# Optimization experiments

Hardware: AMD Instinct MI355X
Metric: run time of the kernel (lower is better)

Reference implementation:

```python
import jax, jax.numpy as jnp
import numpy as np
from jax import lax

SIGMA_D = 120.0
SIGMA_R = 1.2
WINDOW = 3
PAD = WINDOW // 2


def _sobel_kernels():
    smooth = jnp.array([1.0, 2.0, 1.0], dtype=jnp.float32) / 4.0
    deriv = jnp.array([1.0, 0.0, -1.0], dtype=jnp.float32)
    Kh = jnp.einsum('i,j,k->ijk', deriv, smooth, smooth)
    Kw = jnp.einsum('i,j,k->ijk', smooth, deriv, smooth)
    Kd = jnp.einsum('i,j,k->ijk', smooth, smooth, deriv)
    # (O=3, I=1, 3, 3, 3)
    return jnp.stack([Kh, Kw, Kd], axis=0)[:, None]


def _spatial_weights():
    r = np.arange(-PAD, PAD + 1)
    offs = np.stack(np.meshgrid(r, r, r, indexing='ij'), axis=-1).reshape(-1, 3).astype(np.float32)
    dist_sq = (offs ** 2).sum(axis=1)
    return jnp.asarray(np.exp(-dist_sq / (2.0 * SIGMA_D ** 2)))


def setup_inputs() -> dict:
    key = jax.random.key(0)
    volume = jax.random.normal(key, (1, 1, 96, 96, 96), dtype=jnp.float32)
    return {"volume": volume}


def reference(volume):
    B, C, D, H, W = volume.shape
    kernels = _sobel_kernels()
    # Sobel gradient, SAME (zero) padding like F.conv3d(padding=1): (B,3,D,H,W)
    grad = lax.conv_general_dilated(
        volume, kernels, window_strides=(1, 1, 1), padding=[(1, 1)] * 3,
        dimension_numbers=('NCDHW', 'OIDHW', 'NCDHW'))

    pad_cfg = ((0, 0), (0, 0), (PAD, PAD), (PAD, PAD), (PAD, PAD))
    vol_pad = jnp.pad(volume, pad_cfg, mode='edge')
    grad_pad = jnp.pad(grad, pad_cfg, mode='edge')

    offsets = [(dh, dw, dd) for dh in range(WINDOW) for dw in range(WINDOW) for dd in range(WINDOW)]
    # (B, K, D, H, W)
    neighbor_vals = jnp.stack(
        [vol_pad[:, 0, dh:dh + D, dw:dw + H, dd:dd + W] for (dh, dw, dd) in offsets], axis=1)
    # (B, K, 3, D, H, W)
    neighbor_grads = jnp.stack(
        [grad_pad[:, :, dh:dh + D, dw:dw + H, dd:dd + W] for (dh, dw, dd) in offsets], axis=1)

    # ||grad_p - grad_q||^2 over the 3 gradient channels; gaussian on the norm
    # equals exp(-||.||^2 / (2 sigma_r^2)) directly (sqrt then square cancels).
    grad_diff_sq = ((grad[:, None] - neighbor_grads) ** 2).sum(axis=2)  # (B,K,D,H,W)
    range_weights = jnp.exp(-grad_diff_sq / (2.0 * SIGMA_R ** 2))

    sw = _spatial_weights().reshape(1, -1, 1, 1, 1)
    weights = sw * range_weights
    numerator = (weights * neighbor_vals).sum(axis=1, keepdims=True)
    denominator = jnp.clip(weights.sum(axis=1, keepdims=True), 1e-8, None)
    return numerator / denominator
```

## Files before the change

### kernel.cpp

```cpp
#include <hip/hip_runtime.h>


#define NV 96
#define NV2 (NV * NV)

#define TX 32
#define TY 4
#define TZ 4
#define VX (TX + 4)
#define VY (TY + 4)
#define VZ (TZ + 4)
#define GX (TX + 2)
#define GY (TY + 2)
#define GZ (TZ + 2)
#define NVOL (VX * VY * VZ)

__global__ __launch_bounds__(256) void fused_bilateral_kernel(
    const float* __restrict__ vol, float* __restrict__ out) {
    __shared__ float sv[VZ][VY][VX];
    __shared__ float4 sq[GZ][GY][GX];

    const int X0 = blockIdx.x * TX;
    const int Y0 = blockIdx.y * TY;
    const int Z0 = blockIdx.z * TZ;
    const int t = threadIdx.x;

    for (int li = t; li < NVOL; li += 256) {
        int lx = li % VX;
        int lyz = li / VX;
        int ly = lyz % VY;
        int lz = lyz / VY;
        int gx = X0 - 2 + lx;
        int gy = Y0 - 2 + ly;
        int gz = Z0 - 2 + lz;
        float v = 0.0f;
        if (gx >= 0 && gx < NV && gy >= 0 && gy < NV && gz >= 0 && gz < NV)
            v = vol[gz * NV2 + gy * NV + gx];
        sv[lz][ly][lx] = v;
    }
    __syncthreads();

    if (t < GX * GY) {
        const int gx_ = t % GX;
        const int gy_ = t / GX;
        float s0 = 0.f, s1 = 0.f, s2 = 0.f;
        float w0 = 0.f, w1 = 0.f, w2 = 0.f;
        float u0 = 0.f, u1 = 0.f, u2 = 0.f;
        float v11p = 0.f;
#pragma unroll
        for (int p = 0; p < VZ; ++p) {
            float a00 = sv[p][gy_ + 0][gx_ + 0];
            float a01 = sv[p][gy_ + 0][gx_ + 1];
            float a02 = sv[p][gy_ + 0][gx_ + 2];
            float a10 = sv[p][gy_ + 1][gx_ + 0];
            float a11 = sv[p][gy_ + 1][gx_ + 1];
            float a12 = sv[p][gy_ + 1][gx_ + 2];
            float a20 = sv[p][gy_ + 2][gx_ + 0];
            float a21 = sv[p][gy_ + 2][gx_ + 1];
            float a22 = sv[p][gy_ + 2][gx_ + 2];
            float r0 = 0.25f * a00 + 0.5f * a01 + 0.25f * a02;
            float r1 = 0.25f * a10 + 0.5f * a11 + 0.25f * a12;
            float r2 = 0.25f * a20 + 0.5f * a21 + 0.25f * a22;
            float sxy = 0.25f * r0 + 0.5f * r1 + 0.25f * r2;
            float dyx = r0 - r2;
            float dx0 = a00 - a02;
            float dx1 = a10 - a12;
            float dx2 = a20 - a22;
            float dxs = 0.25f * dx0 + 0.5f * dx1 + 0.25f * dx2;
            s0 = s1; s1 = s2; s2 = sxy;
            w0 = w1; w1 = w2; w2 = dyx;
            u0 = u1; u1 = u2; u2 = dxs;
            if (p >= 2) {
                float gh = s0 - s2;
                float gw = 0.25f * w0 + 0.5f * w1 + 0.25f * w2;
                float gd = 0.25f * u0 + 0.5f * u1 + 0.25f * u2;
                sq[p - 2][gy_][gx_] = make_float4(gh, gw, gd, v11p);
            }
            v11p = a11;
        }
    }
    __syncthreads();

    const int tx = t & 31;
    const int ty = (t >> 5) & 3;
    const int tzh = t >> 7;

    const float inv2sd = 1.0f / (2.0f * 120.0f * 120.0f);
    const float inv2sr = 1.0f / (2.0f * 1.2f * 1.2f);

    const int ox = X0 + tx;
    const int oy = Y0 + ty;
    const int oz0 = Z0 + tzh;
    const int oz1 = oz0 + 2;

    const float4 c0 = sq[tzh + 1][ty + 1][tx + 1];
    const float4 c1 = sq[tzh + 3][ty + 1][tx + 1];

    int nx[3], ny[3], nz[5];
#pragma unroll
    for (int d = 0; d < 3; ++d) {
        nx[d] = min(max(ox + d - 1, 0), NV - 1) - (X0 - 1);
        ny[d] = min(max(oy + d - 1, 0), NV - 1) - (Y0 - 1);
    }
#pragma unroll
    for (int p = 0; p < 5; ++p)
        nz[p] = min(max(oz0 + p - 1, 0), NV - 1) - (Z0 - 1);

    float num0 = 0.0f, den0 = 0.0f, num1 = 0.0f, den1 = 0.0f;

#pragma unroll
    for (int p = 0; p < 5; ++p) {
#pragma unroll
        for (int iy = 0; iy < 3; ++iy) {
#pragma unroll
            for (int ix = 0; ix < 3; ++ix) {
                float4 q = sq[nz[p]][ny[iy]][nx[ix]];
                if (p <= 2) {
                    const float sdc =
                        (float)((p - 1) * (p - 1) + (iy - 1) * (iy - 1) +
                                (ix - 1) * (ix - 1)) * inv2sd;
                    float a = c0.x - q.x, b = c0.y - q.y, e = c0.z - q.z;
                    float g = a * a + b * b + e * e;
                    float w = __expf(-(sdc + g * inv2sr));
                    num0 += w * q.w;
                    den0 += w;
                }
                if (p >= 2) {
                    const float sdc =
                        (float)((p - 3) * (p - 3) + (iy - 1) * (iy - 1) +
                                (ix - 1) * (ix - 1)) * inv2sd;
                    float a = c1.x - q.x, b = c1.y - q.y, e = c1.z - q.z;
                    float g = a * a + b * b + e * e;
                    float w = __expf(-(sdc + g * inv2sr));
                    num1 += w * q.w;
                    den1 += w;
                }
            }
        }
    }

    out[oz0 * NV2 + oy * NV + ox] = num0 / fmaxf(den0, 1e-8f);
    out[oz1 * NV2 + oy * NV + ox] = num1 / fmaxf(den1, 1e-8f);
}

extern "C" void kernel_launch(void* const* d_in, const int* in_sizes, int n_in,
                              void* d_out, int out_size, void* d_ws, size_t ws_size,
                              hipStream_t stream) {
    const float* vol = (const float*)d_in[0];
    float* out = (float*)d_out;

    dim3 grid(NV / TX, NV / TY, NV / TZ);
    fused_bilateral_kernel<<<grid, dim3(256), 0, stream>>>(vol, out);
}
```

Baseline: 71.20 us.

## Enlarge tile to 32x8x4 and compute four z-outputs per thread

Doubles the tile height so each 256-thread block covers 32x8x4 outputs. Each thread now walks a 6-deep z column of the gradient tile and accumulates four outputs, reusing each shared-memory neighbour load across up to three outputs. It also folds the spatial constant into a single fma feeding a raw exp2 intrinsic, and splits the gradient-column stage into a loop because 340 columns exceed the block size. This cuts halo overhead and LDS reads per output, at the cost of more shared memory and registers per block and half as many blocks.

After: 77.11 us. 1.08x slower.

```diff
diff --git a/kernel.cpp b/kernel.cpp
--- a/kernel.cpp
+++ b/kernel.cpp
@@ -5,7 +5,7 @@
 #define NV2 (NV * NV)
 
 #define TX 32
-#define TY 4
+#define TY 8
 #define TZ 4
 #define VX (TX + 4)
 #define VY (TY + 4)
@@ -14,6 +14,9 @@
 #define GY (TY + 2)
 #define GZ (TZ + 2)
 #define NVOL (VX * VY * VZ)
+#define NCOL (GX * GY)
+
+#define LOG2E 1.44269504088896340736f
 
 __global__ __launch_bounds__(256) void fused_bilateral_kernel(
     const float* __restrict__ vol, float* __restrict__ out) {
@@ -40,107 +43,107 @@
     }
     __syncthreads();
 
-    if (t < GX * GY) {
-        const int gx_ = t % GX;
-        const int gy_ = t / GX;
-        float s0 = 0.f, s1 = 0.f, s2 = 0.f;
-        float w0 = 0.f, w1 = 0.f, w2 = 0.f;
-        float u0 = 0.f, u1 = 0.f, u2 = 0.f;
-        float v11p = 0.f;
 #pragma unroll
-        for (int p = 0; p < VZ; ++p) {
-            float a00 = sv[p][gy_ + 0][gx_ + 0];
-            float a01 = sv[p][gy_ + 0][gx_ + 1];
-            float a02 = sv[p][gy_ + 0][gx_ + 2];
-            float a10 = sv[p][gy_ + 1][gx_ + 0];
-            float a11 = sv[p][gy_ + 1][gx_ + 1];
-            float a12 = sv[p][gy_ + 1][gx_ + 2];
-            float a20 = sv[p][gy_ + 2][gx_ + 0];
-            float a21 = sv[p][gy_ + 2][gx_ + 1];
-            float a22 = sv[p][gy_ + 2][gx_ + 2];
-            float r0 = 0.25f * a00 + 0.5f * a01 + 0.25f * a02;
-            float r1 = 0.25f * a10 + 0.5f * a11 + 0.25f * a12;
-            float r2 = 0.25f * a20 + 0.5f * a21 + 0.25f * a22;
-            float sxy = 0.25f * r0 + 0.5f * r1 + 0.25f * r2;
-            float dyx = r0 - r2;
-            float dx0 = a00 - a02;
-            float dx1 = a10 - a12;
-            float dx2 = a20 - a22;
-            float dxs = 0.25f * dx0 + 0.5f * dx1 + 0.25f * dx2;
-            s0 = s1; s1 = s2; s2 = sxy;
-            w0 = w1; w1 = w2; w2 = dyx;
-            u0 = u1; u1 = u2; u2 = dxs;
-            if (p >= 2) {
-                float gh = s0 - s2;
-                float gw = 0.25f * w0 + 0.5f * w1 + 0.25f * w2;
-                float gd = 0.25f * u0 + 0.5f * u1 + 0.25f * u2;
-                sq[p - 2][gy_][gx_] = make_float4(gh, gw, gd, v11p);
+    for (int base = 0; base < NCOL; base += 256) {
+        int li = base + t;
+        if (li < NCOL) {
+            const int gx_ = li % GX;
+            const int gy_ = li / GX;
+            float s0 = 0.f, s1 = 0.f, s2 = 0.f;
+            float w0 = 0.f, w1 = 0.f, w2 = 0.f;
+            float u0 = 0.f, u1 = 0.f, u2 = 0.f;
+            float v11p = 0.f;
+#pragma unroll
+            for (int p = 0; p < VZ; ++p) {
+                float a00 = sv[p][gy_ + 0][gx_ + 0];
+                float a01 = sv[p][gy_ + 0][gx_ + 1];
+                float a02 = sv[p][gy_ + 0][gx_ + 2];
+                float a10 = sv[p][gy_ + 1][gx_ + 0];
+                float a11 = sv[p][gy_ + 1][gx_ + 1];
+                float a12 = sv[p][gy_ + 1][gx_ + 2];
+                float a20 = sv[p][gy_ + 2][gx_ + 0];
+                float a21 = sv[p][gy_ + 2][gx_ + 1];
+                float a22 = sv[p][gy_ + 2][gx_ + 2];
+                float r0 = 0.25f * a00 + 0.5f * a01 + 0.25f * a02;
+                float r1 = 0.25f * a10 + 0.5f * a11 + 0.25f * a12;
+                float r2 = 0.25f * a20 + 0.5f * a21 + 0.25f * a22;
+                float sxy = 0.25f * r0 + 0.5f * r1 + 0.25f * r2;
+                float dyx = r0 - r2;
+                float dx0 = a00 - a02;
+                float dx1 = a10 - a12;
+                float dx2 = a20 - a22;
+                float dxs = 0.25f * dx0 + 0.5f * dx1 + 0.25f * dx2;
+                s0 = s1; s1 = s2; s2 = sxy;
+                w0 = w1; w1 = w2; w2 = dyx;
+                u0 = u1; u1 = u2; u2 = dxs;
+                if (p >= 2) {
+                    float gh = s0 - s2;
+                    float gw = 0.25f * w0 + 0.5f * w1 + 0.25f * w2;
+                    float gd = 0.25f * u0 + 0.5f * u1 + 0.25f * u2;
+                    sq[p - 2][gy_][gx_] = make_float4(gh, gw, gd, v11p);
+                }
+                v11p = a11;
             }
-            v11p = a11;
         }
     }
     __syncthreads();
 
     const int tx = t & 31;
-    const int ty = (t >> 5) & 3;
-    const int tzh = t >> 7;
-
-    const float inv2sd = 1.0f / (2.0f * 120.0f * 120.0f);
-    const float inv2sr = 1.0f / (2.0f * 1.2f * 1.2f);
-
+    const int ty = t >> 5;
     const int ox = X0 + tx;
     const int oy = Y0 + ty;
-    const int oz0 = Z0 + tzh;
-    const int oz1 = oz0 + 2;
 
-    const float4 c0 = sq[tzh + 1][ty + 1][tx + 1];
-    const float4 c1 = sq[tzh + 3][ty + 1][tx + 1];
+    const float RC = LOG2E / (2.0f * 1.2f * 1.2f);
 
-    int nx[3], ny[3], nz[5];
+    const float4 c0 = sq[1][ty + 1][tx + 1];
+    const float4 c1 = sq[2][ty + 1][tx + 1];
+    const float4 c2 = sq[3][ty + 1][tx + 1];
+    const float4 c3 = sq[4][ty + 1][tx + 1];
+
+    int nx[3], ny[3], nz[6];
 #pragma unroll
     for (int d = 0; d < 3; ++d) {
         nx[d] = min(max(ox + d - 1, 0), NV - 1) - (X0 - 1);
         ny[d] = min(max(oy + d - 1, 0), NV - 1) - (Y0 - 1);
     }
 #pragma unroll
-    for (int p = 0; p < 5; ++p)
-        nz[p] = min(max(oz0 + p - 1, 0), NV - 1) - (Z0 - 1);
+    for (int p = 0; p < 6; ++p)
+        nz[p] = min(max(Z0 + p - 1, 0), NV - 1) - (Z0 - 1);
 
-    float num0 = 0.0f, den0 = 0.0f, num1 = 0.0f, den1 = 0.0f;
+    float num[4] = {0.f, 0.f, 0.f, 0.f};
+    float den[4] = {0.f, 0.f, 0.f, 0.f};
 
 #pragma unroll
-    for (int p = 0; p < 5; ++p) {
+    for (int p = 0; p < 6; ++p) {
 #pragma unroll
         for (int iy = 0; iy < 3; ++iy) {
 #pragma unroll
             for (int ix = 0; ix < 3; ++ix) {
                 float4 q = sq[nz[p]][ny[iy]][nx[ix]];
-                if (p <= 2) {
-                    const float sdc =
-                        (float)((p - 1) * (p - 1) + (iy - 1) * (iy - 1) +
-                                (ix - 1) * (ix - 1)) * inv2sd;
-                    float a = c0.x - q.x, b = c0.y - q.y, e = c0.z - q.z;
-                    float g = a * a + b * b + e * e;
-                    float w = __expf(-(sdc + g * inv2sr));
-                    num0 += w * q.w;
-                    den0 += w;
-                }
-                if (p >= 2) {
-                    const float sdc =
-                        (float)((p - 3) * (p - 3) + (iy - 1) * (iy - 1) +
-                                (ix - 1) * (ix - 1)) * inv2sd;
-                    float a = c1.x - q.x, b = c1.y - q.y, e = c1.z - q.z;
-                    float g = a * a + b * b + e * e;
-                    float w = __expf(-(sdc + g * inv2sr));
-                    num1 += w * q.w;
-                    den1 += w;
+#pragma unroll
+                for (int k = 0; k < 4; ++k) {
+                    const int dz = p - 1 - k;
+                    if (dz >= -1 && dz <= 1) {
+                        const float SDC =
+                            -(float)(dz * dz + (iy - 1) * (iy - 1) +
+                                     (ix - 1) * (ix - 1)) *
+                            (LOG2E / (2.0f * 120.0f * 120.0f));
+                        float4 c = (k == 0) ? c0 : (k == 1) ? c1
+                                 : (k == 2) ? c2 : c3;
+                        float a = c.x - q.x, b = c.y - q.y, e = c.z - q.z;
+                        float g = a * a + b * b + e * e;
+                        float w = __builtin_amdgcn_exp2f(fmaf(-g, RC, SDC));
+                        num[k] += w * q.w;
+                        den[k] += w;
+                    }
                 }
             }
         }
     }
 
-    out[oz0 * NV2 + oy * NV + ox] = num0 / fmaxf(den0, 1e-8f);
-    out[oz1 * NV2 + oy * NV + ox] = num1 / fmaxf(den1, 1e-8f);
+#pragma unroll
+    for (int k = 0; k < 4; ++k)
+        out[(Z0 + k) * NV2 + oy * NV + ox] = num[k] / fmaxf(den[k], 1e-8f);
 }
 
 extern "C" void kernel_launch(void* const* d_in, const int* in_sizes, int n_in,
```
